# Kernel tuning notes

Hardware: AMD Instinct MI355X
Metric: run time of the kernel (lower is better)

## Reference

```python
import jax, jax.numpy as jnp
import numpy as np

B, S, D, E, K = 4, 2048, 1024, 8, 2
EPS, W_THRES, TEMP = 1e-4, 0.1, 1.0


def setup_inputs() -> dict:
    key = jax.random.key(0)
    k1, k2, k3, k4, k5 = jax.random.split(key, 5)
    x = jax.random.normal(k1, (B, S, D), dtype=jnp.float32)
    gate_W = jax.random.normal(k2, (D, E), dtype=jnp.float32) * 0.02
    gate_b = jnp.zeros((E,), dtype=jnp.float32)
    expert_W = jax.random.normal(k3, (E, D, D), dtype=jnp.float32) * 0.02
    expert_b = jnp.zeros((E, D), dtype=jnp.float32)
    return {"x": x, "gate_W": gate_W, "gate_b": gate_b,
            "expert_W": expert_W, "expert_b": expert_b}


def reference(x, gate_W, gate_b, expert_W, expert_b):
    # Gating: linear -> temperature -> clamp-min(eps) -> softmax
    scores = jnp.maximum((x @ gate_W + gate_b) / TEMP, EPS)      # [B,S,E]
    p = jax.nn.softmax(scores, axis=-1)                           # [B,S,E]
    _, topk_idx = jax.lax.top_k(p, K)                             # [B,S,K]
    # boolean membership mask of selected experts
    topk_mask = jax.nn.one_hot(topk_idx, E, dtype=p.dtype).sum(-2) > 0  # [B,S,E]
    # weights: clamp-min(weight_thres), normalized by detached sum over selected
    w = jnp.maximum(p, W_THRES)                                   # [B,S,E]
    w_gather = jnp.take_along_axis(w, topk_idx, axis=-1)          # [B,S,K]
    total = jax.lax.stop_gradient(w_gather.sum(-1, keepdims=True))
    w = w / total
    comb = jnp.where(topk_mask, w, jnp.zeros_like(w))             # [B,S,E]
    # Dense equivalent of gather/expert/scatter loop (E small): each expert
    # is Linear(D, D); masked combine weights zero out unselected experts.
    y = jnp.einsum('bsd,edf->bsef', x, expert_W) + expert_b       # [B,S,E,D]
    out = jnp.einsum('bsef,bse->bsf', y, comb) / K                # [B,S,D]
    return out
```

## Files before the change

kernel.cpp:

```cpp
#include <hip/hip_runtime.h>
#include <stdint.h>

#define TOK 8192
#define DIM 1024
#define NE 8
#define NTILE 136

typedef short bf16x8 __attribute__((ext_vector_type(8)));
typedef float f32x4 __attribute__((ext_vector_type(4)));

__device__ __forceinline__ unsigned short f2bf(float f) {
  unsigned int u = __float_as_uint(f);
  u += 0x7FFFu + ((u >> 16) & 1u);
  return (unsigned short)(u >> 16);
}

__device__ __forceinline__ void gl_lds16(const void* g, void* l) {
  __builtin_amdgcn_global_load_lds(
      (__attribute__((address_space(1))) unsigned int*)(g),
      (__attribute__((address_space(3))) unsigned int*)(l), 16, 0, 0);
}

__global__ __launch_bounds__(256) void gate_kernel(
    const float* __restrict__ x, const float* __restrict__ gW,
    const float* __restrict__ gb, unsigned short* __restrict__ xb,
    int* __restrict__ eSel, float* __restrict__ wSel, int* __restrict__ cnt)
{
  if (blockIdx.x == 0 && threadIdx.x < NE) cnt[threadIdx.x] = 0;

  const int wave = threadIdx.x >> 6;
  const int lane = threadIdx.x & 63;
  const int t = blockIdx.x * 4 + wave;
  const float4* xrow = (const float4*)(x + (size_t)t * DIM);
  ushort4* xbrow = (ushort4*)(xb + (size_t)t * DIM);

  double acc[NE];
#pragma unroll
  for (int e = 0; e < NE; ++e) acc[e] = 0.0;

#pragma unroll
  for (int i = 0; i < 4; ++i) {
    const int j = i * 64 + lane;
    float4 v = xrow[j];
    ushort4 pk;
    pk.x = f2bf(v.x); pk.y = f2bf(v.y); pk.z = f2bf(v.z); pk.w = f2bf(v.w);
    xbrow[j] = pk;
    const float* g = gW + (size_t)j * 4 * NE;
    float xv[4] = {v.x, v.y, v.z, v.w};
#pragma unroll
    for (int c = 0; c < 4; ++c) {
#pragma unroll
      for (int e = 0; e < NE; ++e)
        acc[e] += (double)xv[c] * (double)g[c * NE + e];
    }
  }
#pragma unroll
  for (int off = 32; off > 0; off >>= 1) {
#pragma unroll
    for (int e = 0; e < NE; ++e)
      acc[e] += __shfl_xor(acc[e], off, 64);
  }

  if (lane == 0) {
    double s[NE];
#pragma unroll
    for (int e = 0; e < NE; ++e) {
      s[e] = acc[e] + (double)gb[e];
      if (s[e] < 1e-4) s[e] = 1e-4;
    }
    int e0 = 0;
    for (int e = 1; e < NE; ++e) if (s[e] > s[e0]) e0 = e;
    int e1 = (e0 == 0) ? 1 : 0;
    for (int e = 0; e < NE; ++e) if (e != e0 && s[e] > s[e1]) e1 = e;
    float m = (float)s[e0];
    float Z = 0.f, pf[NE];
#pragma unroll
    for (int e = 0; e < NE; ++e) { pf[e] = __expf((float)s[e] - m); Z += pf[e]; }
    float w0 = pf[e0] / Z; if (w0 < 0.1f) w0 = 0.1f;
    float w1 = pf[e1] / Z; if (w1 < 0.1f) w1 = 0.1f;
    const float inv = 0.5f / (w0 + w1);
    eSel[t * 2 + 0] = e0;
    eSel[t * 2 + 1] = e1;
    wSel[t * 2 + 0] = w0 * inv;
    wSel[t * 2 + 1] = w1 * inv;
  }
}

__global__ __launch_bounds__(256) void scatter_kernel(
    const int* __restrict__ eSel, const float* __restrict__ wSel,
    int* __restrict__ cnt, int* __restrict__ listTok, float* __restrict__ listW)
{
  __shared__ int lcnt[NE];
  __shared__ int base[NE];
  const int tid = threadIdx.x;
  if (tid < NE) lcnt[tid] = 0;
  __syncthreads();

  const int t = blockIdx.x * 256 + tid;
  const int e0 = eSel[t * 2 + 0];
  const int e1 = eSel[t * 2 + 1];
  const float w0 = wSel[t * 2 + 0];
  const float w1 = wSel[t * 2 + 1];
  const int l0 = atomicAdd(&lcnt[e0], 1);
  const int l1 = atomicAdd(&lcnt[e1], 1);
  __syncthreads();
  if (tid < NE) base[tid] = atomicAdd(&cnt[tid], lcnt[tid]);
  __syncthreads();

  const int p0 = base[e0] + l0;
  listTok[e0 * TOK + p0] = t * 2 + 0;
  listW [e0 * TOK + p0] = w0;
  const int p1 = base[e1] + l1;
  listTok[e1 * TOK + p1] = t * 2 + 1;
  listW [e1 * TOK + p1] = w1;
}

__global__ __launch_bounds__(256) void transpose_w(
    const float* __restrict__ W, unsigned short* __restrict__ Wt)
{
  __shared__ float t[32 * 17 + 16];
  const int e  = blockIdx.x >> 6;
  const int fb = blockIdx.x & 63;
  const int f0 = fb * 16;
  const int tid = threadIdx.x;
  const float* Wb = W + (size_t)e * DIM * DIM + f0;
  unsigned short* Ob = Wt + ((size_t)(e * 64 + fb) * 32) * 512;

  for (int kc = 0; kc < 32; ++kc) {
    const int d0 = kc * 32;
    __syncthreads();
#pragma unroll
    for (int h = 0; h < 512; h += 256) {
      const int idx = tid + h;
      t[(idx >> 4) * 17 + (idx & 15)] = Wb[(size_t)(d0 + (idx >> 4)) * DIM + (idx & 15)];
    }
    __syncthreads();
#pragma unroll
    for (int h = 0; h < 512; h += 256) {
      const int o = tid + h;
      Ob[(size_t)kc * 512 + o] = f2bf(t[(o & 31) * 17 + (o >> 5)]);
    }
  }
}

__global__ __launch_bounds__(256) void moe_gemm(
    const unsigned short* __restrict__ xb, const unsigned short* __restrict__ Wt,
    const float* __restrict__ eb, const int* __restrict__ cnt,
    const int* __restrict__ listTok, const float* __restrict__ listW,
    float* __restrict__ yslot)
{
  const int dId = blockIdx.x % NTILE;
  const int cT  = blockIdx.x / NTILE;
  int e = -1, r0 = 0, rows = 0, accT = 0;
#pragma unroll
  for (int ee = 0; ee < NE; ++ee) {
    const int c = cnt[ee];
    const int nt = (c + 127) >> 7;
    if (dId >= accT && dId < accT + nt) {
      e = ee; r0 = (dId - accT) * 128;
      rows = c - r0; if (rows > 128) rows = 128;
    }
    accT += nt;
  }
  if (e < 0) return;

  __shared__ __align__(16) unsigned short As[2][128 * 32];
  __shared__ int   tid_s[128];
  __shared__ float w_s[128];

  const int tid = threadIdx.x;
  if (tid < 128) {
    if (tid < rows) {
      tid_s[tid] = listTok[e * TOK + r0 + tid];
      w_s[tid]   = listW [e * TOK + r0 + tid];
    } else {
      tid_s[tid] = 0;
      w_s[tid]   = 0.0f;
    }
  }
  __syncthreads();

  const int w    = tid >> 6;
  const int lane = tid & 63;
  const int qsrc = (lane & 3) ^ ((lane >> 3) & 3);
  const int rA0  = w * 32 + (lane >> 2);
  const int rA1  = rA0 + 16;
  const unsigned short* srcA0 = xb + (size_t)(tid_s[rA0] >> 1) * DIM + qsrc * 8;
  const unsigned short* srcA1 = xb + (size_t)(tid_s[rA1] >> 1) * DIM + qsrc * 8;

  const int wr = w >> 1, wc = w & 1;
  const int mrow = lane & 15;
  const int qg   = lane >> 4;
  const int qsA  = (qg ^ ((mrow >> 1) & 3)) * 8;

  const unsigned short* bbase =
      Wt + ((size_t)(e * 64 + cT * 8 + wc * 4) * 32) * 512 + mrow * 32 + qg * 8;

  f32x4 acc[4][4];
#pragma unroll
  for (int i = 0; i < 4; ++i)
#pragma unroll
    for (int j = 0; j < 4; ++j)
      acc[i][j] = {0.f, 0.f, 0.f, 0.f};

  gl_lds16(srcA0, &As[0][w * 1024]);
  gl_lds16(srcA1, &As[0][w * 1024 + 512]);

  for (int kc = 0; kc < DIM / 32; ++kc) {
    const int cur = kc & 1;
    __syncthreads();
    bf16x8 b[4];
#pragma unroll
    for (int nt = 0; nt < 4; ++nt)
      b[nt] = *(const bf16x8*)(bbase + (size_t)nt * 16384 + kc * 512);
    if (kc < DIM / 32 - 1) {
      const int k1 = (kc + 1) * 32;
      unsigned short* a = &As[cur ^ 1][w * 1024];
      gl_lds16(srcA0 + k1, a);
      gl_lds16(srcA1 + k1, a + 512);
    }
    bf16x8 af[4];
#pragma unroll
    for (int mt = 0; mt < 4; ++mt)
      af[mt] = *(const bf16x8*)&As[cur][(wr * 64 + mt * 16 + mrow) * 32 + qsA];
#pragma unroll
    for (int nt = 0; nt < 4; ++nt)
#pragma unroll
      for (int mt = 0; mt < 4; ++mt)
        acc[mt][nt] = __builtin_amdgcn_mfma_f32_16x16x32_bf16(
            af[mt], b[nt], acc[mt][nt], 0, 0, 0);
  }

  const int colBase = cT * 128 + wc * 64 + mrow;
  float bias[4];
#pragma unroll
  for (int nt = 0; nt < 4; ++nt)
    bias[nt] = eb[(size_t)e * DIM + colBase + nt * 16];
#pragma unroll
  for (int mt = 0; mt < 4; ++mt) {
#pragma unroll
    for (int r = 0; r < 4; ++r) {
      const int rloc = wr * 64 + mt * 16 + (lane >> 4) * 4 + r;
      if (rloc < rows) {
        const int tk    = tid_s[rloc];
        const float wgt = w_s[rloc];
        float* dst = yslot + ((size_t)(tk & 1) * TOK + (size_t)(tk >> 1)) * DIM;
#pragma unroll
        for (int nt = 0; nt < 4; ++nt)
          dst[colBase + nt * 16] = wgt * (acc[mt][nt][r] + bias[nt]);
      }
    }
  }
}

__global__ __launch_bounds__(256) void combine(
    const float4* __restrict__ y0, const float4* __restrict__ y1,
    float4* __restrict__ out)
{
  const size_t i = (size_t)blockIdx.x * 256 + threadIdx.x;
  float4 a = y0[i], b = y1[i];
  float4 o;
  o.x = a.x + b.x; o.y = a.y + b.y; o.z = a.z + b.z; o.w = a.w + b.w;
  out[i] = o;
}

extern "C" void kernel_launch(void* const* d_in, const int* in_sizes, int n_in,
                              void* d_out, int out_size, void* d_ws, size_t ws_size,
                              hipStream_t stream)
{
  const float* x  = (const float*)d_in[0];
  const float* gW = (const float*)d_in[1];
  const float* gb = (const float*)d_in[2];
  const float* eW = (const float*)d_in[3];
  const float* eb = (const float*)d_in[4];
  float* out = (float*)d_out;

  char* p = (char*)d_ws;
  unsigned short* xb = (unsigned short*)p;  p += (size_t)TOK * DIM * 2;
  unsigned short* Wt = (unsigned short*)p;  p += (size_t)NE * DIM * DIM * 2;
  float* yslot = (float*)p;                 p += (size_t)2 * TOK * DIM * 4;
  int* cnt = (int*)p;                       p += 256;
  int* listTok = (int*)p;                   p += (size_t)NE * TOK * 4;
  float* listW = (float*)p;                 p += (size_t)NE * TOK * 4;

  int*   eSel = (int*)yslot;
  float* wSel = (float*)(yslot + TOK * 2);

  gate_kernel<<<TOK / 4, 256, 0, stream>>>(x, gW, gb, xb, eSel, wSel, cnt);
  scatter_kernel<<<TOK / 256, 256, 0, stream>>>(eSel, wSel, cnt, listTok, listW);
  transpose_w<<<NE * 64, 256, 0, stream>>>(eW, Wt);
  moe_gemm<<<NTILE * 8, 256, 0, stream>>>(xb, Wt, eb, cnt, listTok, listW, yslot);
  combine<<<TOK * DIM / 4 / 256, 256, 0, stream>>>(
      (const float4*)yslot, (const float4*)yslot + (size_t)TOK * DIM / 4, (float4*)out);
}
```

Baseline: 233.2 us.

## Unroll MoE GEMM K-loop by two with register double-buffered B fragments

The k-loop is unrolled by two so the B fragments read from global memory are prefetched one step ahead into alternating register sets. This hides global load latency behind the MFMA work. The block index mapping is also swapped so the eight column tiles of one row tile are adjacent, which should let concurrently scheduled blocks share the same A rows in cache. The cost is higher register pressure from the extra B buffer, which could lower occupancy.

```diff
diff --git a/kernel.cpp b/kernel.cpp
--- a/kernel.cpp
+++ b/kernel.cpp
@@ -149,8 +149,8 @@
     const int* __restrict__ listTok, const float* __restrict__ listW,
     float* __restrict__ yslot)
 {
-  const int dId = blockIdx.x % NTILE;
-  const int cT  = blockIdx.x / NTILE;
+  const int dId = blockIdx.x >> 3;
+  const int cT  = blockIdx.x & 7;
   int e = -1, r0 = 0, rows = 0, accT = 0;
 #pragma unroll
   for (int ee = 0; ee < NE; ++ee) {
@@ -193,8 +193,11 @@
   const int qg   = lane >> 4;
   const int qsA  = (qg ^ ((mrow >> 1) & 3)) * 8;
 
-  const unsigned short* bbase =
-      Wt + ((size_t)(e * 64 + cT * 8 + wc * 4) * 32) * 512 + mrow * 32 + qg * 8;
+  const unsigned short* pB[4];
+#pragma unroll
+  for (int nt = 0; nt < 4; ++nt)
+    pB[nt] = Wt + ((size_t)(e * 64 + cT * 8 + wc * 4 + nt) * 32) * 512
+                + mrow * 32 + qg * 8;
 
   f32x4 acc[4][4];
 #pragma unroll
@@ -203,32 +206,53 @@
     for (int j = 0; j < 4; ++j)
       acc[i][j] = {0.f, 0.f, 0.f, 0.f};
 
+  bf16x8 b0[4], b1[4];
+#pragma unroll
+  for (int nt = 0; nt < 4; ++nt) { b0[nt] = *(const bf16x8*)pB[nt]; pB[nt] += 512; }
   gl_lds16(srcA0, &As[0][w * 1024]);
   gl_lds16(srcA1, &As[0][w * 1024 + 512]);
 
-  for (int kc = 0; kc < DIM / 32; ++kc) {
-    const int cur = kc & 1;
+  for (int kc = 0; kc < DIM / 32; kc += 2) {
     __syncthreads();
-    bf16x8 b[4];
-#pragma unroll
-    for (int nt = 0; nt < 4; ++nt)
-      b[nt] = *(const bf16x8*)(bbase + (size_t)nt * 16384 + kc * 512);
-    if (kc < DIM / 32 - 1) {
+#pragma unroll
+    for (int nt = 0; nt < 4; ++nt) { b1[nt] = *(const bf16x8*)pB[nt]; pB[nt] += 512; }
+    {
       const int k1 = (kc + 1) * 32;
-      unsigned short* a = &As[cur ^ 1][w * 1024];
-      gl_lds16(srcA0 + k1, a);
-      gl_lds16(srcA1 + k1, a + 512);
-    }
-    bf16x8 af[4];
-#pragma unroll
-    for (int mt = 0; mt < 4; ++mt)
-      af[mt] = *(const bf16x8*)&As[cur][(wr * 64 + mt * 16 + mrow) * 32 + qsA];
-#pragma unroll
-    for (int nt = 0; nt < 4; ++nt)
+      gl_lds16(srcA0 + k1, &As[1][w * 1024]);
+      gl_lds16(srcA1 + k1, &As[1][w * 1024 + 512]);
+    }
+    {
+      bf16x8 af[4];
 #pragma unroll
       for (int mt = 0; mt < 4; ++mt)
-        acc[mt][nt] = __builtin_amdgcn_mfma_f32_16x16x32_bf16(
-            af[mt], b[nt], acc[mt][nt], 0, 0, 0);
+        af[mt] = *(const bf16x8*)&As[0][(wr * 64 + mt * 16 + mrow) * 32 + qsA];
+#pragma unroll
+      for (int nt = 0; nt < 4; ++nt)
+#pragma unroll
+        for (int mt = 0; mt < 4; ++mt)
+          acc[mt][nt] = __builtin_amdgcn_mfma_f32_16x16x32_bf16(
+              af[mt], b0[nt], acc[mt][nt], 0, 0, 0);
+    }
+    __syncthreads();
+    if (kc + 2 < DIM / 32) {
+#pragma unroll
+      for (int nt = 0; nt < 4; ++nt) { b0[nt] = *(const bf16x8*)pB[nt]; pB[nt] += 512; }
+      const int k2 = (kc + 2) * 32;
+      gl_lds16(srcA0 + k2, &As[0][w * 1024]);
+      gl_lds16(srcA1 + k2, &As[0][w * 1024 + 512]);
+    }
+    {
+      bf16x8 af[4];
+#pragma unroll
+      for (int mt = 0; mt < 4; ++mt)
+        af[mt] = *(const bf16x8*)&As[1][(wr * 64 + mt * 16 + mrow) * 32 + qsA];
+#pragma unroll
+      for (int nt = 0; nt < 4; ++nt)
+#pragma unroll
+        for (int mt = 0; mt < 4; ++mt)
+          acc[mt][nt] = __builtin_amdgcn_mfma_f32_16x16x32_bf16(
+              af[mt], b1[nt], acc[mt][nt], 0, 0, 0);
+    }
   }
 
   const int colBase = cT * 128 + wc * 64 + mrow;
```

Measured after the change: 253.9 us. 8.9% more time.
